# Kernel optimization log

Hardware: AMD Instinct MI355X
Metric: run time of the kernel (lower is better)

The kernel has to match this reference:

```python
import jax, jax.numpy as jnp
import numpy as np
from jax import lax

NUM_CLASSES = 5
K_MAX = 5
PROTO_DIM = 32
MARGIN = 1.0
ANCHOR_STRENGTH = 1.0
LAMBDA_COMPACT = 0.1
MAX_ANCHORS = 2048
KMEANS_ITERS = 5
EPS = 1e-12


def _normalize(x, axis=-1):
    return x / jnp.sqrt(jnp.sum(x * x, axis=axis, keepdims=True) + EPS)


def _cdist(a, b):
    # Euclidean distance matrix (n, m) via the squared-norm expansion.
    d2 = (jnp.sum(a * a, 1)[:, None] + jnp.sum(b * b, 1)[None, :] - 2.0 * (a @ b.T))
    return jnp.sqrt(jnp.maximum(d2, 0.0))


def _class_centroids(feats, mask, key):
    # feats: (N, D) L2-normalized; mask: (N,) bool selecting this class's voxels.
    N, D = feats.shape
    w = mask.astype(feats.dtype)
    cnt = w.sum()
    mean = (feats * w[:, None]).sum(0) / jnp.maximum(cnt, 1.0)

    def kmeans(_):
        k_init, k_fb = jax.random.split(key)
        # random init: K distinct masked points (gumbel top-k == randperm sample)
        g0 = jax.random.gumbel(k_init, (N,))
        _, init_idx = lax.top_k(jnp.where(mask, g0, -jnp.inf), K_MAX)
        cent0 = feats[init_idx]
        # fallback random masked points for empty clusters, one set per iter
        g2 = jax.random.gumbel(k_fb, (KMEANS_ITERS, N))
        fb_idx = jax.vmap(lambda s: lax.top_k(jnp.where(mask, s, -jnp.inf), K_MAX)[1])(g2)

        def body(cent, fb):
            d = _cdist(feats, cent)                       # (N, K)
            assign = jnp.argmin(d, axis=1)
            onehot = ((assign[:, None] == jnp.arange(K_MAX)[None, :]) & mask[:, None]).astype(feats.dtype)
            counts = onehot.sum(0)                        # (K,)
            sums = onehot.T @ feats                       # (K, D)
            newc = sums / jnp.maximum(counts, 1.0)[:, None]
            newc = jnp.where(counts[:, None] > 0, newc, feats[fb])
            return newc, None

        cent, _ = lax.scan(body, cent0, fb_idx)
        return _normalize(cent)

    def mean_rep(_):
        return jnp.tile(mean[None, :], (K_MAX, 1))

    cent = lax.cond(cnt >= K_MAX, kmeans, mean_rep, None)
    return _normalize(cent), cnt


def _loss_triplet(feats, prototypes, pseudo_masks, gt_masks, labeled_batch):
    B, Df, Zf, Yf, Xf = feats.shape
    N = B * Zf * Yf * Xf
    feats_flat = _normalize(jnp.transpose(feats, (0, 2, 3, 4, 1)).reshape(N, Df))
    # masks are already at feature resolution -> nearest interp is identity
    gt_flat = gt_masks.reshape(-1)
    pseudo_flat = pseudo_masks.reshape(-1)
    protos = _normalize(prototypes)                       # (C, K, D)
    key = jax.random.key(42)

    # ---- anchor loss: match prototypes to per-class kmeans centroids ----
    anchor_loss = jnp.float32(0.0)
    anchor_cnt = jnp.float32(0.0)
    for i in range(int(labeled_batch.shape[0])):
        c = labeled_batch[i]
        c_safe = jnp.clip(c, 0, NUM_CLASSES - 1)
        cmask = gt_flat == c
        cent, cnt = _class_centroids(feats_flat, cmask, jax.random.fold_in(key, i))
        valid = ((c != 0) & (c < NUM_CLASSES) & (cnt > 0)).astype(jnp.float32)
        loss_c = jnp.mean((protos[c_safe] - cent) ** 2)
        anchor_loss = anchor_loss + valid * loss_c
        anchor_cnt = anchor_cnt + valid
    anchor_loss = anchor_loss / jnp.maximum(anchor_cnt, 1.0)

    # ---- compactness: unbiased variance across the K prototypes per class ----
    compact_loss = jnp.var(protos[1:], axis=1, ddof=1).mean(axis=1).sum()

    # ---- triplet loss over pseudo-labeled anchors ----
    amask = pseudo_flat > 0
    ga = jax.random.gumbel(jax.random.fold_in(key, 1000), (N,))
    top_s, aidx = lax.top_k(jnp.where(amask, ga, -jnp.inf), MAX_ANCHORS)
    sel_valid = jnp.isfinite(top_s)                        # padding if < MAX_ANCHORS anchors
    a_feats = feats_flat[aidx]                             # (A, D)
    a_labels = jnp.clip(pseudo_flat[aidx], 0, NUM_CLASSES - 1)

    CK = NUM_CLASSES * K_MAX
    protos_flat = protos.reshape(CK, Df)
    col_cls = jnp.arange(CK) // K_MAX
    own = col_cls[None, :] == a_labels[:, None]            # (A, CK)

    sim = a_feats @ protos_flat.T
    pos_idx = jnp.argmax(jnp.where(own, sim, -jnp.inf), axis=1)
    pos_vecs = protos_flat[pos_idx]

    d_all = _cdist(a_feats, protos_flat)                   # (A, CK)
    pos_d = jnp.min(jnp.where(own, d_all, jnp.inf), axis=1)
    neg = ~own
    semi = neg & (d_all > pos_d[:, None]) & (d_all < pos_d[:, None] + MARGIN)
    g1 = jax.random.gumbel(jax.random.fold_in(key, 2000), (MAX_ANCHORS, CK))
    g2 = jax.random.gumbel(jax.random.fold_in(key, 2001), (MAX_ANCHORS, CK))
    idx_semi = jnp.argmax(jnp.where(semi, g1, -jnp.inf), axis=1)
    idx_rand = jnp.argmax(jnp.where(neg, g2, -jnp.inf), axis=1)
    neg_idx = jnp.where(semi.any(axis=1), idx_semi, idx_rand)
    neg_vecs = protos_flat[neg_idx]

    aN, pN, nN = _normalize(a_feats), _normalize(pos_vecs), _normalize(neg_vecs)
    d_pos = jnp.sqrt(jnp.sum((aN - pN) ** 2, axis=1) + EPS)
    d_neg = jnp.sqrt(jnp.sum((aN - nN) ** 2, axis=1) + EPS)
    wA = (sel_valid & (a_labels != 0)).astype(jnp.float32)
    proto_loss = jnp.sum(jax.nn.softplus(d_pos - d_neg + MARGIN) * wA) / jnp.maximum(wA.sum(), 1.0)

    return proto_loss + ANCHOR_STRENGTH * anchor_loss + LAMBDA_COMPACT * compact_loss


def setup_inputs() -> dict:
    key = jax.random.key(0)
    k1, k2, k3, k4 = jax.random.split(key, 4)
    B, Z = 4, 64
    feats = jax.random.normal(k1, (B, PROTO_DIM, Z, Z, Z), dtype=jnp.float32)
    protos = jax.random.normal(k2, (NUM_CLASSES, K_MAX, PROTO_DIM), dtype=jnp.float32)
    protos = _normalize(protos)
    pseudo_masks = jax.random.randint(k3, (B, Z, Z, Z), 0, NUM_CLASSES, dtype=jnp.int32)
    gt_masks = jax.random.randint(k4, (B, Z, Z, Z), 0, NUM_CLASSES, dtype=jnp.int32)
    labeled_batch = jnp.array([1, 2, 3, 4], dtype=jnp.int32)
    return {"feats": feats, "prototypes": protos, "pseudo_masks": pseudo_masks,
            "gt_masks": gt_masks, "labeled_batch": labeled_batch}


def reference(feats, prototypes, pseudo_masks, gt_masks, labeled_batch):
    return _loss_triplet(feats, prototypes, pseudo_masks, gt_masks, labeled_batch)
```

## Files before the change

kernel.cpp:

```cpp
#include <hip/hip_runtime.h>
#include <stdint.h>

typedef unsigned int u32;
typedef unsigned long long u64;

#define NCLS 5
#define KMX 5
#define DD 32
#define LBN 4
#define KIT 5
#define MAXA 2048
#define CKK 25
#define NBLKA 256
#define SCPAD 36
#define PSTRIDE 680
#define ACAP 4096
#define UKTHR ((1u << 23) + 1u - (1u << 15))
#define FTINY 1.17549435e-38f

struct RKeys {
  u32 ki[LBN][2];
  u32 kf[LBN][2];
  u32 k1000[2];
  u32 k2000[2];
  u32 k2001[2];
};

struct SelState {
  u32 prefix1, rank1, prefix21, rank2, pivot_sv, target, M, ncand, ncand2;
};

__host__ __device__ inline void tf2x32(u32 k0, u32 k1, u32 x0, u32 x1, u32* o0, u32* o1) {
  u32 ks2 = k0 ^ k1 ^ 0x1BD11BDAu;
  u32 ks[3] = {k0, k1, ks2};
  x0 += k0; x1 += k1;
  const int rotA[4] = {13, 15, 26, 6};
  const int rotB[4] = {17, 29, 16, 24};
#pragma unroll
  for (int g = 0; g < 5; ++g) {
#pragma unroll
    for (int j = 0; j < 4; ++j) {
      int r = (g & 1) ? rotB[j] : rotA[j];
      x0 += x1;
      x1 = (x1 << r) | (x1 >> (32 - r));
      x1 ^= x0;
    }
    x0 += ks[(g + 1) % 3];
    x1 += ks[(g + 2) % 3] + (u32)(g + 1);
  }
  *o0 = x0; *o1 = x1;
}

__device__ inline u32 jax_ukey(u32 k0, u32 k1, u32 half, u32 idx) {
  bool hi = (idx >= half);
  u32 c0 = hi ? (idx - half) : idx;
  u32 c1 = hi ? idx : (idx + half);
  u32 o0, o1;
  tf2x32(k0, k1, c0, c1, &o0, &o1);
  u32 bits = hi ? o1 : o0;
  return (bits >> 9) + 1u;
}

#define INS5(kk, a0, a1, a2, a3, a4) do { u64 _k = (kk); \
  if (_k > a4) { a4 = _k; u64 _t; \
    if (a4 > a3) { _t = a3; a3 = a4; a4 = _t; } \
    if (a3 > a2) { _t = a2; a2 = a3; a3 = _t; } \
    if (a2 > a1) { _t = a1; a1 = a2; a2 = _t; } \
    if (a1 > a0) { _t = a0; a0 = a1; a1 = _t; } } } while (0)

#define WMERGE5(off, a0, a1, a2, a3, a4) do { \
  u64 r0 = __shfl_xor(a0, off, 64), r1 = __shfl_xor(a1, off, 64), \
      r2 = __shfl_xor(a2, off, 64), r3 = __shfl_xor(a3, off, 64), \
      r4 = __shfl_xor(a4, off, 64); \
  INS5(r0, a0, a1, a2, a3, a4); INS5(r1, a0, a1, a2, a3, a4); \
  INS5(r2, a0, a1, a2, a3, a4); INS5(r3, a0, a1, a2, a3, a4); \
  INS5(r4, a0, a1, a2, a3, a4); } while (0)

#define WMERGE_ALL(a0,a1,a2,a3,a4) do { \
  WMERGE5(32,a0,a1,a2,a3,a4); WMERGE5(16,a0,a1,a2,a3,a4); WMERGE5(8,a0,a1,a2,a3,a4); \
  WMERGE5(4,a0,a1,a2,a3,a4); WMERGE5(2,a0,a1,a2,a3,a4); WMERGE5(1,a0,a1,a2,a3,a4); } while (0)

__device__ inline float rsum32(float v) {
#pragma unroll
  for (int o = 16; o; o >>= 1) v += __shfl_xor(v, o, 32);
  return v;
}

__device__ inline float rsum64(float v) {
#pragma unroll
  for (int o = 32; o; o >>= 1) v += __shfl_xor(v, o, 64);
  return v;
}


__global__ void k_protos(const float* __restrict__ protos, float* __restrict__ protn, float* __restrict__ compact) {
  __shared__ float pl[CKK * DD];
  __shared__ float rn[CKK];
  __shared__ float red[4];
  int tid = threadIdx.x;
  for (int t = tid; t < CKK * DD; t += 256) pl[t] = protos[t];
  __syncthreads();
  if (tid < CKK) {
    float s = 0.f;
    for (int d = 0; d < DD; ++d) { float x = pl[tid * DD + d]; s += x * x; }
    rn[tid] = sqrtf(s + 1e-12f);
  }
  __syncthreads();
  for (int t = tid; t < CKK * DD; t += 256) {
    float v = pl[t] / rn[t / DD];
    pl[t] = v;
    protn[t] = v;
  }
  __syncthreads();
  float part = 0.f;
  if (tid < (NCLS - 1) * DD) {
    int c = 1 + tid / DD;
    int d = tid % DD;
    float m = 0.f;
#pragma unroll
    for (int k = 0; k < KMX; ++k) m += pl[(c * KMX + k) * DD + d];
    m *= (1.0f / KMX);
    float v = 0.f;
#pragma unroll
    for (int k = 0; k < KMX; ++k) { float df = pl[(c * KMX + k) * DD + d] - m; v += df * df; }
    part = v * (1.0f / (KMX - 1)) * (1.0f / DD);
  }
#pragma unroll
  for (int o = 32; o; o >>= 1) part += __shfl_xor(part, o, 64);
  int wid = tid >> 6;
  if ((tid & 63) == 0) red[wid] = part;
  __syncthreads();
  if (tid == 0) compact[0] = red[0] + red[1] + red[2] + red[3];
}


#define T5PROC_THR(gv_, nn_) do { \
  int ci = (gv_ == lb0) ? 0 : (gv_ == lb1) ? 1 : (gv_ == lb2) ? 2 : (gv_ == lb3) ? 3 : -1; \
  if (ci >= 0) { \
    u32 k0 = (ci & 2) ? ((ci & 1) ? ka3 : ka2) : ((ci & 1) ? ka1 : ka0); \
    u32 k1 = (ci & 2) ? ((ci & 1) ? kb3 : kb2) : ((ci & 1) ? kb1 : kb0); \
    u32 uk = jax_ukey(k0, k1, half, (u32)(nn_)); \
    if (uk >= UKTHR) { \
      u64 key = ((u64)uk << 32) | (u32)(~(u32)(nn_)); \
      if (ci == 0) { INS5(key, A0, A1, A2, A3, A4); } \
      else if (ci == 1) { INS5(key, B0, B1, B2, B3, B4); } \
      else if (ci == 2) { INS5(key, C0, C1, C2, C3, C4); } \
      else { INS5(key, D0, D1, D2, D3, D4); } \
    } \
  } } while (0)

#define T5PROC(gv_, nn_) do { \
  int ci = (gv_ == lb0) ? 0 : (gv_ == lb1) ? 1 : (gv_ == lb2) ? 2 : (gv_ == lb3) ? 3 : -1; \
  if (ci >= 0) { \
    u32 k0 = (ci & 2) ? ((ci & 1) ? ka3 : ka2) : ((ci & 1) ? ka1 : ka0); \
    u32 k1 = (ci & 2) ? ((ci & 1) ? kb3 : kb2) : ((ci & 1) ? kb1 : kb0); \
    u32 uk = jax_ukey(k0, k1, half, (u32)(nn_)); \
    u64 key = ((u64)uk << 32) | (u32)(~(u32)(nn_)); \
    if (ci == 0) { INS5(key, A0, A1, A2, A3, A4); } \
    else if (ci == 1) { INS5(key, B0, B1, B2, B3, B4); } \
    else if (ci == 2) { INS5(key, C0, C1, C2, C3, C4); } \
    else { INS5(key, D0, D1, D2, D3, D4); } \
  } } while (0)

#define T5_TAIL_STORE() \
  WMERGE_ALL(A0,A1,A2,A3,A4); \
  WMERGE_ALL(B0,B1,B2,B3,B4); \
  WMERGE_ALL(C0,C1,C2,C3,C4); \
  WMERGE_ALL(D0,D1,D2,D3,D4); \
  __shared__ u64 wbuf[4][20]; \
  int tid = threadIdx.x; \
  int wid = tid >> 6; \
  if ((tid & 63) == 0) { \
    u64* w = wbuf[wid]; \
    w[0]=A0; w[1]=A1; w[2]=A2; w[3]=A3; w[4]=A4; \
    w[5]=B0; w[6]=B1; w[7]=B2; w[8]=B3; w[9]=B4; \
    w[10]=C0; w[11]=C1; w[12]=C2; w[13]=C3; w[14]=C4; \
    w[15]=D0; w[16]=D1; w[17]=D2; w[18]=D3; w[19]=D4; \
  } \
  __syncthreads(); \
  if (tid == 0) { \
    _Pragma("unroll") \
    for (int w = 1; w < 4; ++w) { \
      _Pragma("unroll") \
      for (int j = 0; j < 5; ++j) { \
        u64 ka = wbuf[w][j];      INS5(ka, A0, A1, A2, A3, A4); \
        u64 kb = wbuf[w][5 + j];  INS5(kb, B0, B1, B2, B3, B4); \
        u64 kc = wbuf[w][10 + j]; INS5(kc, C0, C1, C2, C3, C4); \
        u64 kd = wbuf[w][15 + j]; INS5(kd, D0, D1, D2, D3, D4); \
      } \
    } \
    size_t nb = gridDim.x; \
    u64* o0 = outA + ((size_t)0 * nb + blockIdx.x) * 5; \
    o0[0]=A0; o0[1]=A1; o0[2]=A2; o0[3]=A3; o0[4]=A4; \
    u64* o1 = outA + ((size_t)1 * nb + blockIdx.x) * 5; \
    o1[0]=B0; o1[1]=B1; o1[2]=B2; o1[3]=B3; o1[4]=B4; \
    u64* o2 = outA + ((size_t)2 * nb + blockIdx.x) * 5; \
    o2[0]=C0; o2[1]=C1; o2[2]=C2; o2[3]=C3; o2[4]=C4; \
    u64* o3 = outA + ((size_t)3 * nb + blockIdx.x) * 5; \
    o3[0]=D0; o3[1]=D1; o3[2]=D2; o3[3]=D3; o3[4]=D4; \
  }

#define T5_HEAD() \
  int lb0 = labeled[0], lb1 = labeled[1], lb2 = labeled[2], lb3 = labeled[3]; \
  u32 half = (u32)(N / 2); \
  u32 ka0 = RK.ki[0][0], kb0 = RK.ki[0][1]; \
  u32 ka1 = RK.ki[1][0], kb1 = RK.ki[1][1]; \
  u32 ka2 = RK.ki[2][0], kb2 = RK.ki[2][1]; \
  u32 ka3 = RK.ki[3][0], kb3 = RK.ki[3][1]; \
  u64 A0=0,A1=0,A2=0,A3=0,A4=0; \
  u64 B0=0,B1=0,B2=0,B3=0,B4=0; \
  u64 C0=0,C1=0,C2=0,C3=0,C4=0; \
  u64 D0=0,D1=0,D2=0,D3=0,D4=0;

__global__ void k_top5A(const int* __restrict__ gt, const int* __restrict__ labeled,
                        RKeys RK, u64* __restrict__ outA, int N) {
  T5_HEAD()
  int Nq = N >> 2;
  int stride = gridDim.x * blockDim.x;
  for (int q = blockIdx.x * blockDim.x + threadIdx.x; q < Nq; q += stride) {
    int4 g4 = ((const int4*)gt)[q];
    int n = q << 2;
    T5PROC_THR(g4.x, n);
    T5PROC_THR(g4.y, n + 1);
    T5PROC_THR(g4.z, n + 2);
    T5PROC_THR(g4.w, n + 3);
  }
  T5_TAIL_STORE()
}

__global__ void k_top5B(const u64* __restrict__ outA, u32* __restrict__ rescue,
                        u64* __restrict__ top5F, int nblk) {
  int i = blockIdx.x;
  const u64* src = outA + (size_t)i * nblk * 5;
  u64 t0 = 0, t1 = 0, t2 = 0, t3 = 0, t4 = 0;
  int tot = nblk * 5;
  for (int j = threadIdx.x; j < tot; j += blockDim.x) { u64 k = src[j]; INS5(k, t0, t1, t2, t3, t4); }
  WMERGE_ALL(t0, t1, t2, t3, t4);
  __shared__ u64 wbuf[4 * 5];
  int tid = threadIdx.x;
  int wid = tid >> 6;
  if ((tid & 63) == 0) {
    wbuf[wid * 5 + 0] = t0; wbuf[wid * 5 + 1] = t1; wbuf[wid * 5 + 2] = t2;
    wbuf[wid * 5 + 3] = t3; wbuf[wid * 5 + 4] = t4;
  }
  __syncthreads();
  if (tid == 0) {
#pragma unroll
    for (int w = 1; w < 4; ++w)
#pragma unroll
      for (int j = 0; j < 5; ++j) { u64 k = wbuf[w * 5 + j]; INS5(k, t0, t1, t2, t3, t4); }
    u64* o = top5F + (size_t)i * 5;
    o[0] = t0; o[1] = t1; o[2] = t2; o[3] = t3; o[4] = t4;
    if (t4 == 0ULL) atomicOr(rescue, 1u << i);
  }
}

__global__ void k_top5A_resc(const int* __restrict__ gt, const int* __restrict__ labeled,
                             RKeys RK, const u32* __restrict__ rescue,
                             u64* __restrict__ outA, int N) {
  if ((rescue[0] & 0xFu) == 0u) return;
  T5_HEAD()
  int Nq = N >> 2;
  int stride = gridDim.x * blockDim.x;
  for (int q = blockIdx.x * blockDim.x + threadIdx.x; q < Nq; q += stride) {
    int4 g4 = ((const int4*)gt)[q];
    int n = q << 2;
    T5PROC(g4.x, n);
    T5PROC(g4.y, n + 1);
    T5PROC(g4.z, n + 2);
    T5PROC(g4.w, n + 3);
  }
  T5_TAIL_STORE()
}

__global__ void k_top5B_resc(const u64* __restrict__ outA, const u32* __restrict__ rescue,
                             u64* __restrict__ top5F, int nblk) {
  int i = blockIdx.x;
  if (!((rescue[0] >> i) & 1u)) return;
  const u64* src = outA + (size_t)i * nblk * 5;
  u64 t0 = 0, t1 = 0, t2 = 0, t3 = 0, t4 = 0;
  int tot = nblk * 5;
  for (int j = threadIdx.x; j < tot; j += blockDim.x) { u64 k = src[j]; INS5(k, t0, t1, t2, t3, t4); }
  WMERGE_ALL(t0, t1, t2, t3, t4);
  __shared__ u64 wbuf[4 * 5];
  int tid = threadIdx.x;
  int wid = tid >> 6;
  if ((tid & 63) == 0) {
    wbuf[wid * 5 + 0] = t0; wbuf[wid * 5 + 1] = t1; wbuf[wid * 5 + 2] = t2;
    wbuf[wid * 5 + 3] = t3; wbuf[wid * 5 + 4] = t4;
  }
  __syncthreads();
  if (tid == 0) {
#pragma unroll
    for (int w = 1; w < 4; ++w)
#pragma unroll
      for (int j = 0; j < 5; ++j) { u64 k = wbuf[w * 5 + j]; INS5(k, t0, t1, t2, t3, t4); }
    u64* o = top5F + (size_t)i * 5;
    o[0] = t0; o[1] = t1; o[2] = t2; o[3] = t3; o[4] = t4;
  }
}


__global__ void __launch_bounds__(256)
k_normT(const float4* __restrict__ feats4, float4* __restrict__ featsN4, int N, int Z3) {
  __shared__ float xl[128 * 33];
  __shared__ float sinv[128];
  int tid = threadIdx.x;
  int nchunk = N >> 7;
  int Z3q = Z3 >> 2;
  for (int chunk = blockIdx.x; chunk < nchunk; chunk += gridDim.x) {
    int n0 = chunk << 7;
    int b = n0 / Z3, v0 = n0 - b * Z3;
    const float4* fb4 = feats4 + (size_t)b * DD * Z3q + (v0 >> 2);
#pragma unroll
    for (int j = 0; j < 4; ++j) {
      int idx = j * 256 + tid;
      int d = idx >> 5, v4 = idx & 31;
      float4 f = fb4[(size_t)d * Z3q + v4];
      int vb = v4 << 2;
      xl[(vb + 0) * 33 + d] = f.x;
      xl[(vb + 1) * 33 + d] = f.y;
      xl[(vb + 2) * 33 + d] = f.z;
      xl[(vb + 3) * 33 + d] = f.w;
    }
    __syncthreads();
    if (tid < 128) {
      float s = 0.f;
#pragma unroll
      for (int d = 0; d < DD; ++d) { float x = xl[tid * 33 + d]; s += x * x; }
      sinv[tid] = 1.0f / sqrtf(s + 1e-12f);
    }
    __syncthreads();
#pragma unroll
    for (int j = 0; j < 4; ++j) {
      int idx = j * 256 + tid;
      int vox = idx >> 3, q = idx & 7;
      float iv = sinv[vox];
      float4 o;
      o.x = xl[vox * 33 + q * 4 + 0] * iv;
      o.y = xl[vox * 33 + q * 4 + 1] * iv;
      o.z = xl[vox * 33 + q * 4 + 2] * iv;
      o.w = xl[vox * 33 + q * 4 + 3] * iv;
      featsN4[(size_t)n0 * 8 + idx] = o;
    }
    __syncthreads();
  }
}

__global__ void k_initcentT(const float* __restrict__ featsN,
                            const u64* __restrict__ top5F, float* __restrict__ cent, int N) {
  int t = threadIdx.x;
  if (t >= LBN * KMX * DD) return;
  int d = t & 31;
  int k = (t >> 5) % KMX;
  int i = t / (KMX * DD);
  u32 n = ~(u32)(top5F[(size_t)i * 5 + k]);
  if (n >= (u32)N) n = 0;
  cent[(i * KMX + k) * DD + d] = featsN[(size_t)n * DD + d];
}

__global__ void __launch_bounds__(256)
k_assignW2(const float4* __restrict__ featsN4, const int* __restrict__ gt,
           const int* __restrict__ labeled, const float* __restrict__ cent,
           float* __restrict__ part, int N) {
  __shared__ float sc[LBN * KMX * SCPAD];
  __shared__ float ssw[8][LBN * KMX * SCPAD];
  __shared__ float scn[LBN * KMX];
  __shared__ float scw[8][LBN * KMX];
  int tid = threadIdx.x;
  for (int t = tid; t < LBN * KMX * DD; t += 256) {
    int cl2 = t >> 5, d = t & 31;
    sc[cl2 * SCPAD + d] = cent[t];
  }
  for (int t = tid; t < 8 * LBN * KMX * SCPAD; t += 256) (&ssw[0][0])[t] = 0.f;
  for (int t = tid; t < 8 * LBN * KMX; t += 256) (&scw[0][0])[t] = 0.f;
  __syncthreads();
  if (tid < LBN * KMX) {
    float s = 0.f;
#pragma unroll
    for (int d = 0; d < DD; ++d) { float c = sc[tid * SCPAD + d]; s += c * c; }
    scn[tid] = s;
  }
  __syncthreads();
  int lb0 = labeled[0], lb1 = labeled[1], lb2 = labeled[2], lb3 = labeled[3];
  int q = tid & 7;
  int grp = (tid >> 3) & 7;
  int wv = tid >> 6;
  int cpi = 2 * wv + (grp >> 2);
  float* myss = &ssw[cpi][0];
  float* mysc = &scw[cpi][0];
  int sstep = grp & 3;
  const float* scq = sc + q * 4;
  int nchunk = N >> 5;
  int chunk = blockIdx.x;
  if (chunk < nchunk) {
    float4 f4 = featsN4[(size_t)chunk * 256 + tid];
    int g = gt[(chunk << 5) + (tid >> 3)];
    while (true) {
      int nxt = chunk + gridDim.x;
      bool has = nxt < nchunk;
      float4 nf4; int ng = 0;
      if (has) {
        nf4 = featsN4[(size_t)nxt * 256 + tid];
        ng = gt[(nxt << 5) + (tid >> 3)];
      }
      int ci = (g == lb0) ? 0 : (g == lb1) ? 1 : (g == lb2) ? 2 : (g == lb3) ? 3 : -1;
      int basec = (ci < 0 ? 0 : ci) * KMX;
      float4 c0 = *(const float4*)(scq + (basec + 0) * SCPAD);
      float4 c1 = *(const float4*)(scq + (basec + 1) * SCPAD);
      float4 c2 = *(const float4*)(scq + (basec + 2) * SCPAD);
      float4 c3 = *(const float4*)(scq + (basec + 3) * SCPAD);
      float4 c4 = *(const float4*)(scq + (basec + 4) * SCPAD);
      float p0 = f4.x * c0.x + f4.y * c0.y + f4.z * c0.z + f4.w * c0.w;
      float p1 = f4.x * c1.x + f4.y * c1.y + f4.z * c1.z + f4.w * c1.w;
      float p2 = f4.x * c2.x + f4.y * c2.y + f4.z * c2.z + f4.w * c2.w;
      float p3 = f4.x * c3.x + f4.y * c3.y + f4.z * c3.z + f4.w * c3.w;
      float p4 = f4.x * c4.x + f4.y * c4.y + f4.z * c4.z + f4.w * c4.w;
#pragma unroll
      for (int o = 1; o < 8; o <<= 1) {
        p0 += __shfl_xor(p0, o, 64);
        p1 += __shfl_xor(p1, o, 64);
        p2 += __shfl_xor(p2, o, 64);
        p3 += __shfl_xor(p3, o, 64);
        p4 += __shfl_xor(p4, o, 64);
      }
      float bd = scn[basec + 0] - 2.0f * p0; int bk = 0;
      float d2;
      d2 = scn[basec + 1] - 2.0f * p1; if (d2 < bd) { bd = d2; bk = 1; }
      d2 = scn[basec + 2] - 2.0f * p2; if (d2 < bd) { bd = d2; bk = 2; }
      d2 = scn[basec + 3] - 2.0f * p3; if (d2 < bd) { bd = d2; bk = 3; }
      d2 = scn[basec + 4] - 2.0f * p4; if (d2 < bd) { bd = d2; bk = 4; }
      int cl = basec + bk;
#pragma unroll
      for (int s = 0; s < 4; ++s) {
        if (sstep == s && ci >= 0) {
          float* dst = myss + cl * SCPAD + q * 4;
          float4 cur = *(float4*)dst;
          cur.x += f4.x; cur.y += f4.y; cur.z += f4.z; cur.w += f4.w;
          *(float4*)dst = cur;
          if (q == 0) mysc[cl] += 1.0f;
        }
      }
      if (!has) break;
      chunk = nxt; f4 = nf4; g = ng;
    }
  }
  __syncthreads();
  float* po = part + (size_t)blockIdx.x * PSTRIDE;
  for (int p = tid; p < 660; p += 256) {
    float v;
    if (p < 640) {
      int idx = (p >> 5) * SCPAD + (p & 31);
      v = ssw[0][idx] + ssw[1][idx] + ssw[2][idx] + ssw[3][idx]
        + ssw[4][idx] + ssw[5][idx] + ssw[6][idx] + ssw[7][idx];
    } else {
      int ik = p - 640;
      v = scw[0][ik] + scw[1][ik] + scw[2][ik] + scw[3][ik]
        + scw[4][ik] + scw[5][ik] + scw[6][ik] + scw[7][ik];
    }
    po[p] = v;
  }
}

__global__ void k_redupdT(const float* __restrict__ part, float* __restrict__ cent,
                          float* __restrict__ sums, float* __restrict__ kcnt,
                          u32* __restrict__ emptyMask, int NB) {
  __shared__ float w4[8];
  int p = blockIdx.x;
  int tid = threadIdx.x;
  if (p < 640) {
    int ik = p >> 5;
    float s = 0.f, c = 0.f;
    for (int b2 = tid; b2 < NB; b2 += 256) {
      s += part[(size_t)b2 * PSTRIDE + p];
      c += part[(size_t)b2 * PSTRIDE + 640 + ik];
    }
    s = rsum64(s); c = rsum64(c);
    int wid = tid >> 6;
    if ((tid & 63) == 0) { w4[wid] = s; w4[4 + wid] = c; }
    __syncthreads();
    if (tid == 0) {
      float S = w4[0] + w4[1] + w4[2] + w4[3];
      float C = w4[4] + w4[5] + w4[6] + w4[7];
      sums[p] = S;
      if (C > 0.f) cent[p] = S / fmaxf(C, 1.0f);
      else atomicOr(emptyMask, 1u << ik);
    }
  } else if (p < 660) {
    int ik = p - 640;
    float c = 0.f;
    for (int b2 = tid; b2 < NB; b2 += 256) c += part[(size_t)b2 * PSTRIDE + 640 + ik];
    c = rsum64(c);
    int wid = tid >> 6;
    if ((tid & 63) == 0) w4[wid] = c;
    __syncthreads();
    if (tid == 0) kcnt[ik] = w4[0] + w4[1] + w4[2] + w4[3];
  }
}

__global__ void __launch_bounds__(1024)
k_fixempty(const float* __restrict__ featsN, const int* __restrict__ gt,
           const int* __restrict__ labeled, RKeys RK, u32* __restrict__ emptyMask,
           float* __restrict__ cent, int iter, int N) {
  u32 mask = emptyMask[0];
  if (mask == 0u) return;
  __shared__ u64 wbuf[16 * 5];
  __shared__ u32 idxs[KMX];
  int tid = threadIdx.x;
  u32 halfF = (u32)(((u64)5 * (u64)N) / 2);
  for (int ci = 0; ci < LBN; ++ci) {
    if (((mask >> (ci * KMX)) & 0x1Fu) == 0u) continue;
    int c = labeled[ci];
    u32 fa = RK.kf[ci][0], fb = RK.kf[ci][1];
    u32 base = (u32)iter * (u32)N;
    u64 t0 = 0, t1 = 0, t2 = 0, t3 = 0, t4 = 0;
    for (int n = tid; n < N; n += 1024) {
      if (gt[n] != c) continue;
      u32 uk = jax_ukey(fa, fb, halfF, base + (u32)n);
      u64 key = ((u64)uk << 32) | (u32)(~(u32)n);
      INS5(key, t0, t1, t2, t3, t4);
    }
    WMERGE_ALL(t0, t1, t2, t3, t4);
    int wid = tid >> 6;
    if ((tid & 63) == 0) {
      wbuf[wid * 5 + 0] = t0; wbuf[wid * 5 + 1] = t1; wbuf[wid * 5 + 2] = t2;
      wbuf[wid * 5 + 3] = t3; wbuf[wid * 5 + 4] = t4;
    }
    __syncthreads();
    if (tid == 0) {
      for (int w = 1; w < 16; ++w)
        for (int j = 0; j < 5; ++j) { u64 k = wbuf[w * 5 + j]; INS5(k, t0, t1, t2, t3, t4); }
      idxs[0] = ~(u32)t0; idxs[1] = ~(u32)t1; idxs[2] = ~(u32)t2;
      idxs[3] = ~(u32)t3; idxs[4] = ~(u32)t4;
    }
    __syncthreads();
    if (tid < KMX * DD) {
      int k = tid >> 5, d = tid & 31;
      if ((mask >> (ci * KMX + k)) & 1u) {
        u32 n = idxs[k];
        if (n >= (u32)N) n = 0;
        cent[(ci * KMX + k) * DD + d] = featsN[(size_t)n * DD + d];
      }
    }
    __syncthreads();
  }
  if (tid == 0) emptyMask[0] = 0u;
}

__global__ void k_prepT(const float4* __restrict__ featsN4,
                        const int* __restrict__ pseudo, const SelState* __restrict__ st,
                        const int* __restrict__ aidx, float4* __restrict__ afe4,
                        int* __restrict__ alab, int N) {
  int tid = threadIdx.x;
  int r = blockIdx.x * 32 + (tid >> 3);
  int q = tid & 7;
  if (r >= (int)st->target) return;
  int n = aidx[r];
  if ((u32)n >= (u32)N) n = 0;
  if (q == 0) {
    int lb = pseudo[n];
    alab[r] = lb < 0 ? 0 : (lb > NCLS - 1 ? NCLS - 1 : lb);
  }
  afe4[(size_t)r * 8 + q] = featsN4[(size_t)n * 8 + q];
}


__global__ void __launch_bounds__(256)
k_anchsel(const int* __restrict__ pseudo, RKeys RK, u64* __restrict__ cand4k,
          SelState* st, int N) {
  __shared__ u32 mcnt[4];
  u32 K0 = RK.k1000[0], K1 = RK.k1000[1];
  u32 half = (u32)(N / 2);
  int tid = threadIdx.x;
  int lcnt = 0;
  int stride = gridDim.x * blockDim.x;
  for (int n = blockIdx.x * blockDim.x + tid; n < N; n += stride) {
    bool valid = pseudo[n] > 0;
    lcnt += valid ? 1 : 0;
    u32 uk = jax_ukey(K0, K1, half, (u32)n);
    bool c = valid && (uk >= UKTHR);
    if (__ballot(c)) {
      if (c) {
        u32 p = atomicAdd(&st->ncand, 1u);
        if (p < (u32)ACAP) cand4k[p] = ((u64)uk << 32) | (u32)(~(u32)n);
      }
    }
  }
#pragma unroll
  for (int o = 32; o; o >>= 1) lcnt += __shfl_xor(lcnt, o, 64);
  if ((tid & 63) == 0) mcnt[tid >> 6] = (u32)lcnt;
  __syncthreads();
  if (tid == 0) atomicAdd(&st->M, mcnt[0] + mcnt[1] + mcnt[2] + mcnt[3]);
}

__global__ void k_selmode(SelState* st, u32* rescue) {
  if (threadIdx.x != 0 || blockIdx.x != 0) return;
  u32 M = st->M;
  u32 tgt = M < (u32)MAXA ? M : (u32)MAXA;
  st->target = tgt;
  if (!(st->ncand >= tgt && st->ncand <= (u32)ACAP)) rescue[1] = 1u;
}

__global__ void __launch_bounds__(256)
k_rank(const u64* __restrict__ cand4k, const SelState* __restrict__ st,
       const u32* __restrict__ rescue, int* __restrict__ aidx) {
  if (rescue[1]) return;
  __shared__ u64 keys[ACAP];
  u32 nc = st->ncand; if (nc > (u32)ACAP) nc = (u32)ACAP;
  u32 target = st->target;
  int tid = threadIdx.x;
  for (int t = tid; t < ACAP; t += 256) keys[t] = (t < (int)nc) ? cand4k[t] : 0ULL;
  __syncthreads();
  int i = blockIdx.x * 256 + tid;
  if (i >= (int)nc) return;
  u64 my = keys[i];
  u32 rank = 0;
  for (u32 j = 0; j < nc; ++j) rank += (keys[j] > my) ? 1u : 0u;
  if (rank < target) aidx[rank] = (int)(~(u32)my);
}


__global__ void k_svinit(const int* __restrict__ pseudo, RKeys RK, const u32* __restrict__ rescue,
                         u32* __restrict__ sv, u32* __restrict__ hist, int N) {
  if (!rescue[1]) return;
  __shared__ u32 h[2048];
  for (int t = threadIdx.x; t < 2048; t += blockDim.x) h[t] = 0;
  __syncthreads();
  u32 half = (u32)(N / 2);
  u32 K0 = RK.k1000[0], K1 = RK.k1000[1];
  int Nq = N >> 2;
  int stride = gridDim.x * blockDim.x;
  for (int q = blockIdx.x * blockDim.x + threadIdx.x; q < Nq; q += stride) {
    int4 p4 = ((const int4*)pseudo)[q];
    int n = q << 2;
    u32 s0 = 0, s1 = 0, s2 = 0, s3 = 0;
    if (p4.x > 0) { s0 = jax_ukey(K0, K1, half, (u32)n);     atomicAdd(&h[s0 >> 21], 1u); }
    if (p4.y > 0) { s1 = jax_ukey(K0, K1, half, (u32)n + 1); atomicAdd(&h[s1 >> 21], 1u); }
    if (p4.z > 0) { s2 = jax_ukey(K0, K1, half, (u32)n + 2); atomicAdd(&h[s2 >> 21], 1u); }
    if (p4.w > 0) { s3 = jax_ukey(K0, K1, half, (u32)n + 3); atomicAdd(&h[s3 >> 21], 1u); }
    ((uint4*)sv)[q] = make_uint4(s0, s1, s2, s3);
  }
  __syncthreads();
  for (int t = threadIdx.x; t < 2048; t += blockDim.x) if (h[t]) atomicAdd(&hist[t], h[t]);
}

__global__ void k_hist12(const u32* __restrict__ sv, u32* __restrict__ hist,
                         const SelState* __restrict__ st, const u32* __restrict__ rescue,
                         int pass, int N) {
  if (!rescue[1]) return;
  __shared__ u32 h[2048];
  for (int t = threadIdx.x; t < 2048; t += blockDim.x) h[t] = 0;
  __syncthreads();
  u32 pre = (pass == 1) ? st->prefix1 : st->prefix21;
  int Nq = N >> 2;
  int stride = gridDim.x * blockDim.x;
  for (int q = blockIdx.x * blockDim.x + threadIdx.x; q < Nq; q += stride) {
    uint4 s4 = ((const uint4*)sv)[q];
#define H12(s_) do { u32 s = (s_); if (s) { \
      if (pass == 1) { if ((s >> 21) == pre) atomicAdd(&h[(s >> 10) & 0x7FFu], 1u); } \
      else           { if ((s >> 10) == pre) atomicAdd(&h[s & 0x3FFu], 1u); } } } while (0)
    H12(s4.x); H12(s4.y); H12(s4.z); H12(s4.w);
#undef H12
  }
  __syncthreads();
  for (int t = threadIdx.x; t < 2048; t += blockDim.x) if (h[t]) atomicAdd(&hist[t], h[t]);
}

__global__ void k_scan(const u32* __restrict__ hist, SelState* st,
                       const u32* __restrict__ rescue, int pass) {
  if (!rescue[1]) return;
  __shared__ u32 h[2048];
  __shared__ u32 csum[256];
  __shared__ u32 sh_rank;
  __shared__ int sh_found;
  __shared__ u32 sh_rem;
  int tid = threadIdx.x;
  int nb = (pass == 2) ? 1024 : 2048;
  for (int t = tid; t < 2048; t += 256) h[t] = (t < nb) ? hist[t] : 0u;
  __syncthreads();
  u32 cs = 0;
#pragma unroll
  for (int j = 0; j < 8; ++j) cs += h[tid * 8 + j];
  csum[tid] = cs;
  __syncthreads();
  if (tid == 0) {
    sh_rank = (pass == 0) ? st->target : (pass == 1 ? st->rank1 : st->rank2);
    sh_found = -1;
    sh_rem = 0;
  }
  __syncthreads();
  u32 rank = sh_rank;
  if (rank > 0) {
    u32 above = 0;
    for (int j = tid + 1; j < 256; ++j) above += csum[j];
    u32 run = above;
    for (int b = tid * 8 + 7; b >= tid * 8; --b) {
      u32 c = h[b];
      if (run < rank && rank <= run + c) { sh_found = b; sh_rem = rank - run; }
      run += c;
    }
  }
  __syncthreads();
  if (tid == 0) {
    int found = sh_found;
    u32 rem = sh_rem;
    if (pass == 0) {
      if (found < 0) { st->prefix1 = 0xFFFFFFFFu; st->rank1 = 0; }
      else { st->prefix1 = (u32)found; st->rank1 = rem; }
    } else if (pass == 1) {
      if (found < 0) { st->prefix21 = 0xFFFFFFFFu; st->rank2 = 0; }
      else { st->prefix21 = (st->prefix1 << 11) | (u32)found; st->rank2 = rem; }
    } else {
      if (found < 0) st->pivot_sv = 0xFFFFFFFFu;
      else st->pivot_sv = (st->prefix21 << 10) | (u32)found;
    }
  }
}

__global__ void k_gather(const u32* __restrict__ sv, SelState* st,
                         const u32* __restrict__ rescue, u64* __restrict__ cand, int N) {
  if (!rescue[1]) return;
  if (st->target == 0) return;
  u32 piv = st->pivot_sv;
  int Nq = N >> 2;
  int stride = gridDim.x * blockDim.x;
  for (int q = blockIdx.x * blockDim.x + threadIdx.x; q < Nq; q += stride) {
    uint4 s4 = ((const uint4*)sv)[q];
    int n = q << 2;
#define GPUSH(s_, nn_) do { u32 s = (s_); \
    if (s && s >= piv) { u32 p = atomicAdd(&st->ncand2, 1u); \
      if (p < 4096u) cand[p] = ((u64)s << 32) | (u32)(~(u32)(nn_)); } } while (0)
    GPUSH(s4.x, n); GPUSH(s4.y, n + 1); GPUSH(s4.z, n + 2); GPUSH(s4.w, n + 3);
#undef GPUSH
  }
}

__global__ void __launch_bounds__(1024) k_sortsel(const u64* __restrict__ cand,
                                                  const SelState* __restrict__ st,
                                                  const u32* __restrict__ rescue,
                                                  int* __restrict__ aidx) {
  if (!rescue[1]) return;
  __shared__ u64 s[4096];
  u32 nc = st->ncand2; if (nc > 4096u) nc = 4096u;
  u32 target = st->target;
  for (int t = threadIdx.x; t < 4096; t += blockDim.x) s[t] = (t < (int)nc) ? cand[t] : 0ULL;
  __syncthreads();
  for (u32 ksz = 2; ksz <= 4096; ksz <<= 1) {
    for (u32 j = ksz >> 1; j > 0; j >>= 1) {
      for (u32 idx = threadIdx.x; idx < 4096; idx += blockDim.x) {
        u32 ixj = idx ^ j;
        if (ixj > idx) {
          bool up = (idx & ksz) == 0;
          u64 A = s[idx], B = s[ixj];
          bool sw = up ? (A < B) : (A > B);
          if (sw) { s[idx] = B; s[ixj] = A; }
        }
      }
      __syncthreads();
    }
  }
  for (int t = threadIdx.x; t < MAXA; t += blockDim.x)
    if (t < (int)target) aidx[t] = (int)(~(u32)s[t]);
}


__global__ void k_anchor_final(const float* __restrict__ cent, const float* __restrict__ sums,
                               const float* __restrict__ kcnt, const float* __restrict__ protn,
                               const int* __restrict__ labeled, float* __restrict__ accum) {
  int i = blockIdx.x;
  int d = threadIdx.x;
  if (d >= DD) return;
  int c = labeled[i];
  float cnt = 0.f;
#pragma unroll
  for (int k = 0; k < KMX; ++k) cnt += kcnt[i * KMX + k];
  int cs = c < 0 ? 0 : (c > NCLS - 1 ? NCLS - 1 : c);
  float part = 0.f;
  if (cnt >= (float)KMX) {
#pragma unroll
    for (int k = 0; k < KMX; ++k) {
      float v = cent[(i * KMX + k) * DD + d];
      float s = rsum32(v * v);
      float dn1 = sqrtf(s + 1e-12f);
      float v1 = v / dn1;
      float s2 = rsum32(v1 * v1);
      float dn2 = sqrtf(s2 + 1e-12f);
      float vv = v1 / dn2;
      float df = protn[(cs * KMX + k) * DD + d] - vv;
      part += df * df;
    }
  } else {
    float mv = 0.f;
#pragma unroll
    for (int k = 0; k < KMX; ++k) mv += sums[(i * KMX + k) * DD + d];
    mv /= fmaxf(cnt, 1.0f);
    float s = rsum32(mv * mv);
    float dn = sqrtf(s + 1e-12f);
    float vv = mv / dn;
#pragma unroll
    for (int k = 0; k < KMX; ++k) {
      float df = protn[(cs * KMX + k) * DD + d] - vv;
      part += df * df;
    }
  }
  float ls = rsum32(part) * (1.0f / (KMX * DD));
  bool valid = (c != 0) && (c < NCLS) && (cnt > 0.f);
  if (d == 0 && valid) { atomicAdd(&accum[0], ls); atomicAdd(&accum[1], 1.0f); }
}

__global__ void k_triplet(const float* __restrict__ protn, const float* __restrict__ afe,
                          const int* __restrict__ alab, const SelState* __restrict__ st,
                          RKeys RK, float* __restrict__ acc) {
  __shared__ float pn[CKK * DD];
  __shared__ float spn[CKK];
  int tid = threadIdx.x;
  for (int t = tid; t < CKK * DD; t += blockDim.x) pn[t] = protn[t];
  __syncthreads();
  if (tid < CKK) {
    float s = 0.f;
    for (int d = 0; d < DD; ++d) s += pn[tid * DD + d] * pn[tid * DD + d];
    spn[tid] = s;
  }
  __syncthreads();
  int r = blockIdx.x * blockDim.x + tid;
  if (r >= (int)st->target) return;
  float a[DD]; float sa = 0.f;
#pragma unroll
  for (int d = 0; d < DD; ++d) { a[d] = afe[(size_t)r * DD + d]; sa += a[d] * a[d]; }
  int lab = alab[r];
  int ob = lab * KMX;
  float bs = -3.4e38f; int pidx = ob;
  float pos_d = 3.4e38f;
  for (int k = ob; k < ob + KMX; ++k) {
    float dot = 0.f;
#pragma unroll
    for (int d = 0; d < DD; ++d) dot += a[d] * pn[k * DD + d];
    if (dot > bs) { bs = dot; pidx = k; }
    float d2 = (sa + spn[k]) - 2.0f * dot;
    float dd = sqrtf(fmaxf(d2, 0.f));
    pos_d = fminf(pos_d, dd);
  }
  u32 halfT = (u32)(MAXA * CKK / 2);
  bool any_semi = false;
  u32 bu1 = 0; int k1i = 0;
  u32 bu2 = 0; int k2i = 0;
  for (int k = 0; k < CKK; ++k) {
    if (k / KMX == lab) continue;
    float dot = 0.f;
#pragma unroll
    for (int d = 0; d < DD; ++d) dot += a[d] * pn[k * DD + d];
    float d2 = (sa + spn[k]) - 2.0f * dot;
    float dd = sqrtf(fmaxf(d2, 0.f));
    u32 j = (u32)(r * CKK + k);
    bool semi = (dd > pos_d) && (dd < pos_d + 1.0f);
    if (semi) {
      u32 u1 = jax_ukey(RK.k2000[0], RK.k2000[1], halfT, j);
      any_semi = true;
      if (u1 > bu1) { bu1 = u1; k1i = k; }
    }
    u32 u2 = jax_ukey(RK.k2001[0], RK.k2001[1], halfT, j);
    if (u2 > bu2) { bu2 = u2; k2i = k; }
  }
  int nidx = any_semi ? k1i : k2i;
  float aden = sqrtf(sa + 1e-12f);
  float pden = sqrtf(spn[pidx] + 1e-12f);
  float nden = sqrtf(spn[nidx] + 1e-12f);
  float s1 = 0.f, s2 = 0.f;
#pragma unroll
  for (int d = 0; d < DD; ++d) {
    float an = a[d] / aden;
    float pv = pn[pidx * DD + d] / pden;
    float nv = pn[nidx * DD + d] / nden;
    float t1 = an - pv; s1 += t1 * t1;
    float t2 = an - nv; s2 += t2 * t2;
  }
  float d_pos = sqrtf(s1 + 1e-12f);
  float d_neg = sqrtf(s2 + 1e-12f);
  float xx = (d_pos - d_neg) + 1.0f;
  float l = fmaxf(xx, 0.f) + log1pf(expf(-fabsf(xx)));
  atomicAdd(&acc[0], l);
  atomicAdd(&acc[1], 1.0f);
}

__global__ void k_final(const float* __restrict__ anchor_acc, const float* __restrict__ proto_acc,
                        const float* __restrict__ compact, float* __restrict__ out) {
  if (threadIdx.x != 0 || blockIdx.x != 0) return;
  float al = anchor_acc[0] / fmaxf(anchor_acc[1], 1.0f);
  float pl = proto_acc[0] / fmaxf(proto_acc[1], 1.0f);
  out[0] = pl + 1.0f * al + 0.1f * compact[0];
}


static void host_keys(RKeys* K) {
  const u32 b0 = 0u, b1 = 42u;
  u32 o0, o1;
  for (int i = 0; i < LBN; ++i) {
    u32 f0, f1;
    tf2x32(b0, b1, 0u, (u32)i, &f0, &f1);
    u32 p0, q0, p1, q1;
    tf2x32(f0, f1, 0u, 2u, &p0, &q0);
    tf2x32(f0, f1, 1u, 3u, &p1, &q1);
    K->ki[i][0] = p0; K->ki[i][1] = p1;
    K->kf[i][0] = q0; K->kf[i][1] = q1;
  }
  tf2x32(b0, b1, 0u, 1000u, &o0, &o1); K->k1000[0] = o0; K->k1000[1] = o1;
  tf2x32(b0, b1, 0u, 2000u, &o0, &o1); K->k2000[0] = o0; K->k2000[1] = o1;
  tf2x32(b0, b1, 0u, 2001u, &o0, &o1); K->k2001[0] = o0; K->k2001[1] = o1;
}

extern "C" void kernel_launch(void* const* d_in, const int* in_sizes, int n_in,
                              void* d_out, int out_size, void* d_ws, size_t ws_size,
                              hipStream_t stream) {
  const float* feats = (const float*)d_in[0];
  const float* protos = (const float*)d_in[1];
  const int* pseudo = (const int*)d_in[2];
  const int* gt = (const int*)d_in[3];
  const int* labeled = (const int*)d_in[4];
  float* out = (float*)d_out;

  int N = in_sizes[2];
  int Z3 = N / 4;

  RKeys RK;
  host_keys(&RK);

  const int nbas[3] = {1536, 768, 384};
  for (int attempt = 0; attempt < 3; ++attempt) {
    int NBAS = nbas[attempt];
    char* W = (char*)d_ws;
    size_t off = 0;
    auto alloc = [&](size_t bytes) -> char* {
      char* p = W + off;
      off += (bytes + 255) & ~(size_t)255;
      return p;
    };
    char* zeroBase = W + off;
    u32* hist3 = (u32*)alloc(3 * 2048 * 4);
    SelState* st = (SelState*)alloc(256);
    float* anchor_acc = (float*)alloc(256);
    float* proto_acc = (float*)alloc(256);
    u32* rescue = (u32*)alloc(256);
    size_t zeroBytes = (size_t)((W + off) - zeroBase);
    u64* cand4k = (u64*)alloc((size_t)ACAP * 8);
    u64* outA = (u64*)alloc((size_t)LBN * NBLKA * 5 * 8);
    u64* top5F = (u64*)alloc((size_t)LBN * 5 * 8);
    float* cent = (float*)alloc((size_t)LBN * KMX * DD * 4);
    float* sums = (float*)alloc((size_t)LBN * KMX * DD * 4);
    float* kcnt = (float*)alloc((size_t)LBN * KMX * 4);
    float* protn = (float*)alloc((size_t)CKK * DD * 4);
    float* compact = (float*)alloc(256);
    u32* sv = (u32*)alloc((size_t)N * 4);
    float* part = (float*)alloc((size_t)NBAS * PSTRIDE * 4);
    u64* cand = (u64*)alloc(4096 * 8);
    int* aidx = (int*)alloc((size_t)MAXA * 4);
    int* alab = (int*)alloc((size_t)MAXA * 4);
    float* afe = (float*)alloc((size_t)MAXA * DD * 4);
    float* featsN = (float*)alloc((size_t)N * DD * 4);
    if (ws_size < off) continue;

    hipMemsetAsync(zeroBase, 0, zeroBytes, stream);

    k_protos<<<dim3(1), dim3(256), 0, stream>>>(protos, protn, compact);

    k_top5A<<<dim3(NBLKA), dim3(256), 0, stream>>>(gt, labeled, RK, outA, N);
    k_top5B<<<dim3(LBN), dim3(256), 0, stream>>>(outA, rescue, top5F, NBLKA);
    k_top5A_resc<<<dim3(NBLKA), dim3(256), 0, stream>>>(gt, labeled, RK, rescue, outA, N);
    k_top5B_resc<<<dim3(LBN), dim3(256), 0, stream>>>(outA, rescue, top5F, NBLKA);

    float4* featsN4 = (float4*)featsN;
    k_normT<<<dim3(4096), dim3(256), 0, stream>>>((const float4*)feats, featsN4, N, Z3);
    k_initcentT<<<dim3(1), dim3(LBN * KMX * DD), 0, stream>>>(featsN, top5F, cent, N);
    for (int it = 0; it < KIT; ++it) {
      k_assignW2<<<dim3(NBAS), dim3(256), 0, stream>>>(featsN4, gt, labeled, cent, part, N);
      k_redupdT<<<dim3(660), dim3(256), 0, stream>>>(part, cent, sums, kcnt, rescue + 2, NBAS);
      k_fixempty<<<dim3(1), dim3(1024), 0, stream>>>(featsN, gt, labeled, RK, rescue + 2, cent, it, N);
    }
    k_anchor_final<<<dim3(LBN), dim3(64), 0, stream>>>(cent, sums, kcnt, protn, labeled, anchor_acc);

    k_anchsel<<<dim3(2048), dim3(256), 0, stream>>>(pseudo, RK, cand4k, st, N);
    k_selmode<<<dim3(1), dim3(64), 0, stream>>>(st, rescue);
    k_svinit<<<dim3(1024), dim3(256), 0, stream>>>(pseudo, RK, rescue, sv, hist3, N);
    k_scan<<<dim3(1), dim3(256), 0, stream>>>(hist3, st, rescue, 0);
    k_hist12<<<dim3(1024), dim3(256), 0, stream>>>(sv, hist3 + 2048, st, rescue, 1, N);
    k_scan<<<dim3(1), dim3(256), 0, stream>>>(hist3 + 2048, st, rescue, 1);
    k_hist12<<<dim3(1024), dim3(256), 0, stream>>>(sv, hist3 + 4096, st, rescue, 2, N);
    k_scan<<<dim3(1), dim3(256), 0, stream>>>(hist3 + 4096, st, rescue, 2);
    k_gather<<<dim3(1024), dim3(256), 0, stream>>>(sv, st, rescue, cand, N);
    k_sortsel<<<dim3(1), dim3(1024), 0, stream>>>(cand, st, rescue, aidx);
    k_rank<<<dim3(ACAP / 256), dim3(256), 0, stream>>>(cand4k, st, rescue, aidx);

    k_prepT<<<dim3(MAXA / 32), dim3(256), 0, stream>>>(featsN4, pseudo, st, aidx,
                                                        (float4*)afe, alab, N);
    k_triplet<<<dim3(MAXA / 256), dim3(256), 0, stream>>>(protn, afe, alab, st, RK, proto_acc);

    k_final<<<dim3(1), dim3(64), 0, stream>>>(anchor_acc, proto_acc, compact, out);
    return;
  }
}
```

Measured before the change: 599.0 us.

## Fuse normalization/transpose with first k-means assignment pass

Initial centroids are now computed straight from the raw feature tensor by normalizing the selected voxels in place. That lets the first k-means assignment and partial-sum pass run inside the normalize-and-transpose kernel, while the normalized features are still in registers. The aim is to drop one full read of the normalized feature array and one kernel launch. In exchange, the fused kernel uses more shared memory and only four per-wave accumulator copies instead of eight, and it runs on the assign grid size instead of 4096 blocks.

New measurement: 609.1 us. No clear change (+1.7%).

```diff
diff --git a/kernel.cpp b/kernel.cpp
--- a/kernel.cpp
+++ b/kernel.cpp
@@ -301,11 +301,55 @@
 }
 
 
+__global__ void k_initcentR(const float* __restrict__ feats, const u64* __restrict__ top5F,
+                            float* __restrict__ cent, int N, int Z3) {
+  int t = threadIdx.x;
+  if (t >= LBN * KMX * DD) return;
+  int d = t & 31;
+  int k = (t >> 5) % KMX;
+  int i = t / (KMX * DD);
+  u32 n = ~(u32)(top5F[(size_t)i * 5 + k]);
+  if (n >= (u32)N) n = 0;
+  int b = n / Z3, v = n - b * Z3;
+  const float* fp = feats + (size_t)b * DD * Z3 + v;
+  float sa = 0.f, xd = 0.f;
+#pragma unroll
+  for (int dd = 0; dd < DD; ++dd) { float x = fp[(size_t)dd * Z3]; sa += x * x; if (dd == d) xd = x; }
+  cent[(i * KMX + k) * DD + d] = xd * (1.0f / sqrtf(sa + 1e-12f));
+}
+
 __global__ void __launch_bounds__(256)
-k_normT(const float4* __restrict__ feats4, float4* __restrict__ featsN4, int N, int Z3) {
+k_normA(const float4* __restrict__ feats4, const int* __restrict__ gt,
+        const int* __restrict__ labeled, const float* __restrict__ cent,
+        float4* __restrict__ featsN4, float* __restrict__ part, int N, int Z3) {
   __shared__ float xl[128 * 33];
   __shared__ float sinv[128];
-  int tid = threadIdx.x;
+  __shared__ float sc[LBN * KMX * SCPAD];
+  __shared__ float ssw[4][LBN * KMX * SCPAD];
+  __shared__ float scn[LBN * KMX];
+  __shared__ float scw[4][LBN * KMX];
+  int tid = threadIdx.x;
+  for (int t = tid; t < LBN * KMX * DD; t += 256) {
+    int cl2 = t >> 5, d = t & 31;
+    sc[cl2 * SCPAD + d] = cent[t];
+  }
+  for (int t = tid; t < 4 * LBN * KMX * SCPAD; t += 256) (&ssw[0][0])[t] = 0.f;
+  for (int t = tid; t < 4 * LBN * KMX; t += 256) (&scw[0][0])[t] = 0.f;
+  __syncthreads();
+  if (tid < LBN * KMX) {
+    float s = 0.f;
+#pragma unroll
+    for (int d = 0; d < DD; ++d) { float c = sc[tid * SCPAD + d]; s += c * c; }
+    scn[tid] = s;
+  }
+  __syncthreads();
+  int lb0 = labeled[0], lb1 = labeled[1], lb2 = labeled[2], lb3 = labeled[3];
+  int q = tid & 7;
+  int grp = (tid >> 3) & 7;
+  int wv = tid >> 6;
+  float* myss = &ssw[wv][0];
+  float* mysc = &scw[wv][0];
+  const float* scq = sc + q * 4;
   int nchunk = N >> 7;
   int Z3q = Z3 >> 2;
   for (int chunk = blockIdx.x; chunk < nchunk; chunk += gridDim.x) {
@@ -334,7 +378,7 @@
 #pragma unroll
     for (int j = 0; j < 4; ++j) {
       int idx = j * 256 + tid;
-      int vox = idx >> 3, q = idx & 7;
+      int vox = idx >> 3;
       float iv = sinv[vox];
       float4 o;
       o.x = xl[vox * 33 + q * 4 + 0] * iv;
@@ -342,21 +386,59 @@
       o.z = xl[vox * 33 + q * 4 + 2] * iv;
       o.w = xl[vox * 33 + q * 4 + 3] * iv;
       featsN4[(size_t)n0 * 8 + idx] = o;
+      int g = gt[n0 + vox];
+      int ci = (g == lb0) ? 0 : (g == lb1) ? 1 : (g == lb2) ? 2 : (g == lb3) ? 3 : -1;
+      int basec = (ci < 0 ? 0 : ci) * KMX;
+      float4 c0 = *(const float4*)(scq + (basec + 0) * SCPAD);
+      float4 c1 = *(const float4*)(scq + (basec + 1) * SCPAD);
+      float4 c2 = *(const float4*)(scq + (basec + 2) * SCPAD);
+      float4 c3 = *(const float4*)(scq + (basec + 3) * SCPAD);
+      float4 c4 = *(const float4*)(scq + (basec + 4) * SCPAD);
+      float p0 = o.x * c0.x + o.y * c0.y + o.z * c0.z + o.w * c0.w;
+      float p1 = o.x * c1.x + o.y * c1.y + o.z * c1.z + o.w * c1.w;
+      float p2 = o.x * c2.x + o.y * c2.y + o.z * c2.z + o.w * c2.w;
+      float p3 = o.x * c3.x + o.y * c3.y + o.z * c3.z + o.w * c3.w;
+      float p4 = o.x * c4.x + o.y * c4.y + o.z * c4.z + o.w * c4.w;
+#pragma unroll
+      for (int of = 1; of < 8; of <<= 1) {
+        p0 += __shfl_xor(p0, of, 64);
+        p1 += __shfl_xor(p1, of, 64);
+        p2 += __shfl_xor(p2, of, 64);
+        p3 += __shfl_xor(p3, of, 64);
+        p4 += __shfl_xor(p4, of, 64);
+      }
+      float bd = scn[basec + 0] - 2.0f * p0; int bk = 0;
+      float d2;
+      d2 = scn[basec + 1] - 2.0f * p1; if (d2 < bd) { bd = d2; bk = 1; }
+      d2 = scn[basec + 2] - 2.0f * p2; if (d2 < bd) { bd = d2; bk = 2; }
+      d2 = scn[basec + 3] - 2.0f * p3; if (d2 < bd) { bd = d2; bk = 3; }
+      d2 = scn[basec + 4] - 2.0f * p4; if (d2 < bd) { bd = d2; bk = 4; }
+      int cl = basec + bk;
+#pragma unroll
+      for (int s = 0; s < 8; ++s) {
+        if (grp == s && ci >= 0) {
+          float* dst = myss + cl * SCPAD + q * 4;
+          float4 cur = *(float4*)dst;
+          cur.x += o.x; cur.y += o.y; cur.z += o.z; cur.w += o.w;
+          *(float4*)dst = cur;
+          if (q == 0) mysc[cl] += 1.0f;
+        }
+      }
     }
     __syncthreads();
   }
-}
-
-__global__ void k_initcentT(const float* __restrict__ featsN,
-                            const u64* __restrict__ top5F, float* __restrict__ cent, int N) {
-  int t = threadIdx.x;
-  if (t >= LBN * KMX * DD) return;
-  int d = t & 31;
-  int k = (t >> 5) % KMX;
-  int i = t / (KMX * DD);
-  u32 n = ~(u32)(top5F[(size_t)i * 5 + k]);
-  if (n >= (u32)N) n = 0;
-  cent[(i * KMX + k) * DD + d] = featsN[(size_t)n * DD + d];
+  float* po = part + (size_t)blockIdx.x * PSTRIDE;
+  for (int p = tid; p < 660; p += 256) {
+    float v;
+    if (p < 640) {
+      int idx = (p >> 5) * SCPAD + (p & 31);
+      v = ssw[0][idx] + ssw[1][idx] + ssw[2][idx] + ssw[3][idx];
+    } else {
+      int ik = p - 640;
+      v = scw[0][ik] + scw[1][ik] + scw[2][ik] + scw[3][ik];
+    }
+    po[p] = v;
+  }
 }
 
 __global__ void __launch_bounds__(256)
@@ -968,9 +1050,12 @@
     k_top5B_resc<<<dim3(LBN), dim3(256), 0, stream>>>(outA, rescue, top5F, NBLKA);
 
     float4* featsN4 = (float4*)featsN;
-    k_normT<<<dim3(4096), dim3(256), 0, stream>>>((const float4*)feats, featsN4, N, Z3);
-    k_initcentT<<<dim3(1), dim3(LBN * KMX * DD), 0, stream>>>(featsN, top5F, cent, N);
-    for (int it = 0; it < KIT; ++it) {
+    k_initcentR<<<dim3(1), dim3(LBN * KMX * DD), 0, stream>>>(feats, top5F, cent, N, Z3);
+    k_normA<<<dim3(NBAS), dim3(256), 0, stream>>>((const float4*)feats, gt, labeled, cent,
+                                                   featsN4, part, N, Z3);
+    k_redupdT<<<dim3(660), dim3(256), 0, stream>>>(part, cent, sums, kcnt, rescue + 2, NBAS);
+    k_fixempty<<<dim3(1), dim3(1024), 0, stream>>>(featsN, gt, labeled, RK, rescue + 2, cent, 0, N);
+    for (int it = 1; it < KIT; ++it) {
       k_assignW2<<<dim3(NBAS), dim3(256), 0, stream>>>(featsN4, gt, labeled, cent, part, N);
       k_redupdT<<<dim3(660), dim3(256), 0, stream>>>(part, cent, sums, kcnt, rescue + 2, NBAS);
       k_fixempty<<<dim3(1), dim3(1024), 0, stream>>>(featsN, gt, labeled, RK, rescue + 2, cent, it, N);
```
